# Optimization experiments

Hardware: AMD Instinct MI355X
Metric: run time of the kernel (lower is better)

The kernel has to match this reference:

```python
import jax, jax.numpy as jnp
import numpy as np

D_MODEL = 1024
HEADS = 16
D_HEAD = D_MODEL // HEADS


def setup_inputs() -> dict:
    key = jax.random.key(0)
    ks = jax.random.split(key, 7)
    s = 1.0 / np.sqrt(D_MODEL)
    x = jax.random.normal(ks[0], (4, 2048, D_MODEL), dtype=jnp.float32)
    Wq = jax.random.uniform(ks[1], (D_MODEL, D_MODEL), jnp.float32, -s, s)
    bq = jax.random.uniform(ks[2], (D_MODEL,), jnp.float32, -s, s)
    Wk = jax.random.uniform(ks[3], (D_MODEL, D_MODEL), jnp.float32, -s, s)
    bk = jax.random.uniform(ks[4], (D_MODEL,), jnp.float32, -s, s)
    Wv = jax.random.uniform(ks[5], (D_MODEL, D_MODEL), jnp.float32, -s, s)
    bv = jax.random.uniform(ks[6], (D_MODEL,), jnp.float32, -s, s)
    return {"x": x, "Wq": Wq, "bq": bq, "Wk": Wk, "bk": bk, "Wv": Wv, "bv": bv}


def reference(x, Wq, bq, Wk, bk, Wv, bv):
    B, S, D = x.shape
    # QKV projections, split heads: [B, H, S, Dh]
    def split(t):
        return t.reshape(B, S, HEADS, D_HEAD).transpose(0, 2, 1, 3)
    q = split(x @ Wq + bq)
    k = split(x @ Wk + bk)
    v = split(x @ Wv + bv)
    scores = jnp.einsum('bhqd,bhkd->bhqk', q, k) / np.sqrt(D_HEAD).astype(jnp.float32)
    attn = jax.nn.softmax(scores, axis=-1)
    out = jnp.einsum('bhqk,bhkd->bhqd', attn, v)
    return out.transpose(0, 2, 1, 3).reshape(B, S, D)
```

## Files before the change

kernel.cpp:

```cpp
#include <hip/hip_runtime.h>

typedef _Float16 f16;
typedef __attribute__((ext_vector_type(2))) _Float16 f16x2;
typedef __attribute__((ext_vector_type(2))) __fp16   hf16x2;
typedef __attribute__((ext_vector_type(4))) _Float16 f16x4;
typedef __attribute__((ext_vector_type(8))) _Float16 f16x8;
typedef __attribute__((ext_vector_type(4))) float    f32x4;

#define D_MODEL 1024
#define HEADS   16
#define DH      64
#define SEQ     2048
#define BATCH   4
#define SSCALE  0.1803368801111204f

__device__ __forceinline__ void gload_lds16(const void* g, void* lds) {
  __builtin_amdgcn_global_load_lds(
      (const __attribute__((address_space(1))) unsigned int*)g,
      (__attribute__((address_space(3))) unsigned int*)lds, 16, 0, 0);
}

__global__ __launch_bounds__(256) void prep_kernel(const float* __restrict__ x,
                                                   const float* __restrict__ Wq,
                                                   const float* __restrict__ Wk,
                                                   const float* __restrict__ Wv,
                                                   f16* __restrict__ xb,
                                                   f16* __restrict__ wt) {
  if (blockIdx.x < 8192) {
    int i = blockIdx.x * 256 + threadIdx.x;
    float4 v = ((const float4*)x)[i];
    f16x4 h;
    h[0] = (f16)v.x; h[1] = (f16)v.y; h[2] = (f16)v.z; h[3] = (f16)v.w;
    ((f16x4*)xb)[i] = h;
    return;
  }
  int bid = blockIdx.x - 8192;
  int z = bid >> 8, rem = bid & 255;
  const float* W = z == 0 ? Wq : (z == 1 ? Wk : Wv);
  f16* out = wt + (size_t)z * D_MODEL * D_MODEL;
  __shared__ float tile[64][65];
  int n0 = (rem & 15) * 64, k0 = (rem >> 4) * 64;
  int tx = threadIdx.x & 63, ty = threadIdx.x >> 6;
#pragma unroll
  for (int r = 0; r < 16; ++r)
    tile[ty * 16 + r][tx] = W[(size_t)(k0 + ty * 16 + r) * D_MODEL + n0 + tx];
  __syncthreads();
#pragma unroll
  for (int r = 0; r < 16; ++r)
    out[(size_t)(n0 + ty * 16 + r) * D_MODEL + k0 + tx] = (f16)tile[tx][ty * 16 + r];
}

__global__ __launch_bounds__(256, 3) void qkv_gemm_kernel(
    const f16* __restrict__ xb, const f16* __restrict__ wt_all,
    const float* __restrict__ bq, const float* __restrict__ bk, const float* __restrict__ bv,
    f16* __restrict__ qout, f16* __restrict__ kout, f16* __restrict__ vtout) {
  const int z = blockIdx.z;
  const f16* wt = wt_all + (size_t)z * D_MODEL * D_MODEL;
  const float* bias = z == 0 ? bq : (z == 1 ? bk : bv);
  const int n0 = blockIdx.x * 128, m0 = blockIdx.y * 128;

  __shared__ f16 As[2][128 * 32];
  __shared__ f16 Bs[2][128 * 32];

  const int tid = threadIdx.x;
  const int lane = tid & 63, w = tid >> 6;
  const int quad = lane >> 4, l15 = lane & 15;
  const int wm = w & 1, wn = w >> 1;

  const int pce = (quad ^ ((l15 >> 1) & 3)) * 8;
  const int aoff = wm * 2048 + l15 * 32 + pce;
  const int boff = wn * 2048 + l15 * 32 + pce;

  int srow[2], scl[2];
#pragma unroll
  for (int c = 0; c < 2; ++c) {
    int slot = (w * 2 + c) * 64 + lane;
    srow[c] = slot >> 2;
    scl[c] = (slot & 3) ^ ((srow[c] >> 1) & 3);
  }

  f32x4 acc[4][4];
#pragma unroll
  for (int i = 0; i < 4; ++i)
#pragma unroll
    for (int j = 0; j < 4; ++j) acc[i][j] = (f32x4){0.f, 0.f, 0.f, 0.f};

#pragma unroll
  for (int c = 0; c < 2; ++c) {
    gload_lds16(xb + (size_t)(m0 + srow[c]) * D_MODEL + scl[c] * 8, &As[0][(w * 2 + c) * 512]);
    gload_lds16(wt + (size_t)(n0 + srow[c]) * D_MODEL + scl[c] * 8, &Bs[0][(w * 2 + c) * 512]);
  }

  f16x8 aP[4], bP[4];
  for (int it = 0; it < 32; ++it) {
    const int buf = it & 1;
    __syncthreads();
    if (it < 31) {
      const int kn = (it + 1) * 32;
#pragma unroll
      for (int c = 0; c < 2; ++c) {
        gload_lds16(xb + (size_t)(m0 + srow[c]) * D_MODEL + kn + scl[c] * 8, &As[buf ^ 1][(w * 2 + c) * 512]);
        gload_lds16(wt + (size_t)(n0 + srow[c]) * D_MODEL + kn + scl[c] * 8, &Bs[buf ^ 1][(w * 2 + c) * 512]);
      }
    }
    f16x8 aC[4], bC[4];
#pragma unroll
    for (int mt = 0; mt < 4; ++mt) aC[mt] = *(const f16x8*)(&As[buf][aoff + mt * 512]);
#pragma unroll
    for (int nt = 0; nt < 4; ++nt) bC[nt] = *(const f16x8*)(&Bs[buf][boff + nt * 512]);
    if (it) {
#pragma unroll
      for (int mt = 0; mt < 4; ++mt)
#pragma unroll
        for (int nt = 0; nt < 4; ++nt)
          acc[mt][nt] = __builtin_amdgcn_mfma_f32_16x16x32_f16(aP[mt], bP[nt], acc[mt][nt], 0, 0, 0);
    }
#pragma unroll
    for (int t = 0; t < 4; ++t) { aP[t] = aC[t]; bP[t] = bC[t]; }
  }
#pragma unroll
  for (int mt = 0; mt < 4; ++mt)
#pragma unroll
    for (int nt = 0; nt < 4; ++nt)
      acc[mt][nt] = __builtin_amdgcn_mfma_f32_16x16x32_f16(aP[mt], bP[nt], acc[mt][nt], 0, 0, 0);

  const float sc = (z == 0) ? SSCALE : 1.0f;
  float bcol[4];
#pragma unroll
  for (int nt = 0; nt < 4; ++nt) bcol[nt] = bias[n0 + wn * 64 + nt * 16 + l15];

  if (z < 2) {
    f16* out = (z == 0) ? qout : kout;
#pragma unroll
    for (int mt = 0; mt < 4; ++mt) {
      int mbase = m0 + wm * 64 + mt * 16 + quad * 4;
#pragma unroll
      for (int nt = 0; nt < 4; ++nt) {
        int n = n0 + wn * 64 + nt * 16 + l15;
        int h = n >> 6, dh = n & 63;
#pragma unroll
        for (int r = 0; r < 4; ++r) {
          int m = mbase + r;
          int b = m >> 11, s = m & 2047;
          out[((size_t)(b * HEADS + h) * SEQ + s) * DH + dh] = (f16)((acc[mt][nt][r] + bcol[nt]) * sc);
        }
      }
    }
  } else {
#pragma unroll
    for (int mt = 0; mt < 4; ++mt) {
      int mbase = m0 + wm * 64 + mt * 16 + quad * 4;
      int b = mbase >> 11, seq = mbase & 2047;
      int kt = seq >> 6;
#pragma unroll
      for (int nt = 0; nt < 4; ++nt) {
        int n = n0 + wn * 64 + nt * 16 + l15;
        int h = n >> 6, dh = n & 63;
        f16x4 v;
#pragma unroll
        for (int r = 0; r < 4; ++r) v[r] = (f16)(acc[mt][nt][r] + bcol[nt]);
        int phys = (quad * 2 + (mt >> 1)) ^ (dh & 7);
        size_t off = (((size_t)(b * HEADS + h) * 32 + kt) * 4096) + dh * 64 + phys * 8 + (mt & 1) * 4;
        *(f16x4*)(vtout + off) = v;
      }
    }
  }
}

__global__ __launch_bounds__(256, 2) void attn_kernel(
    const f16* __restrict__ q, const f16* __restrict__ k, const f16* __restrict__ vt,
    float* __restrict__ out) {
  const int bh = blockIdx.x;
  const int s0 = blockIdx.y * 256;
  const int b = bh >> 4, h = bh & 15;
  const int tid = threadIdx.x, lane = tid & 63, w = tid >> 6;
  const int quad = lane >> 4, l15 = lane & 15;

  __shared__ f16 Ks[2][64 * 64];
  __shared__ f16 Vs[2][64 * 64];

  const f16* qbase = q + ((size_t)bh * SEQ + s0 + w * 64) * DH;
  const f16* kbase = k + (size_t)bh * SEQ * DH;
  const f16* vbase = vt + (size_t)bh * DH * SEQ;

  f16x8 qf[4][2];
#pragma unroll
  for (int qt = 0; qt < 4; ++qt)
#pragma unroll
    for (int ks = 0; ks < 2; ++ks)
      qf[qt][ks] = *(const f16x8*)(qbase + (qt * 16 + l15) * DH + ks * 32 + quad * 8);

  int koff[2];
  koff[0] = l15 * 64 + ((quad ^ (l15 & 7)) * 8);
  koff[1] = l15 * 64 + (((4 + quad) ^ (l15 & 7)) * 8);
  int voff2[2];
  voff2[0] = l15 * 64 + (((quad * 2) ^ (l15 & 7)) * 8);
  voff2[1] = l15 * 64 + (((quad * 2 + 1) ^ (l15 & 7)) * 8);

  int srow[2], scl[2];
#pragma unroll
  for (int c = 0; c < 2; ++c) {
    int slot = (w * 2 + c) * 64 + lane;
    srow[c] = slot >> 3;
    scl[c] = (slot & 7) ^ (srow[c] & 7);
  }
  const int vslot = ((w * 2) * 64 + lane) * 8;
  const int vslot2 = ((w * 2 + 1) * 64 + lane) * 8;

  f32x4 lsum4[4];
#pragma unroll
  for (int qt = 0; qt < 4; ++qt) lsum4[qt] = (f32x4){0.f, 0.f, 0.f, 0.f};
  f32x4 o[4][4];
#pragma unroll
  for (int i = 0; i < 4; ++i)
#pragma unroll
    for (int j = 0; j < 4; ++j) o[i][j] = (f32x4){0.f, 0.f, 0.f, 0.f};
  const f32x4 Zero = (f32x4){0.f, 0.f, 0.f, 0.f};

#pragma unroll
  for (int c = 0; c < 2; ++c)
    gload_lds16(kbase + (size_t)srow[c] * DH + scl[c] * 8, &Ks[0][(w * 2 + c) * 512]);
  gload_lds16(vbase + vslot,  &Vs[0][(w * 2) * 512]);
  gload_lds16(vbase + vslot2, &Vs[0][(w * 2 + 1) * 512]);

  for (int kt = 0; kt < SEQ / 64; ++kt) {
    const int buf = kt & 1;
    __syncthreads();
    if (kt < SEQ / 64 - 1) {
      const int kn = (kt + 1) * 64;
#pragma unroll
      for (int c = 0; c < 2; ++c)
        gload_lds16(kbase + (size_t)(kn + srow[c]) * DH + scl[c] * 8, &Ks[buf ^ 1][(w * 2 + c) * 512]);
      gload_lds16(vbase + (kt + 1) * 4096 + vslot,  &Vs[buf ^ 1][(w * 2) * 512]);
      gload_lds16(vbase + (kt + 1) * 4096 + vslot2, &Vs[buf ^ 1][(w * 2 + 1) * 512]);
    }

    f32x4 st[4][4];
#pragma unroll
    for (int mt = 0; mt < 4; ++mt) {
      f16x8 af0 = *(const f16x8*)(&Ks[buf][koff[0] + mt * 1024]);
      f16x8 af1 = *(const f16x8*)(&Ks[buf][koff[1] + mt * 1024]);
#pragma unroll
      for (int qt = 0; qt < 4; ++qt) {
        st[mt][qt] = __builtin_amdgcn_mfma_f32_16x16x32_f16(af0, qf[qt][0], Zero, 0, 0, 0);
        st[mt][qt] = __builtin_amdgcn_mfma_f32_16x16x32_f16(af1, qf[qt][1], st[mt][qt], 0, 0, 0);
      }
    }

    f16x4 pb[4][4];
#pragma unroll
    for (int ks = 0; ks < 4; ++ks)
#pragma unroll
      for (int qt = 0; qt < 4; ++qt) {
        float e0 = __builtin_amdgcn_exp2f(st[ks][qt][0]);
        float e1 = __builtin_amdgcn_exp2f(st[ks][qt][1]);
        float e2 = __builtin_amdgcn_exp2f(st[ks][qt][2]);
        float e3 = __builtin_amdgcn_exp2f(st[ks][qt][3]);
        f32x4 ev = (f32x4){e0, e1, e2, e3};
        lsum4[qt] += ev;
        f16x2 p01 = __builtin_bit_cast(f16x2, __builtin_amdgcn_cvt_pkrtz(e0, e1));
        f16x2 p23 = __builtin_bit_cast(f16x2, __builtin_amdgcn_cvt_pkrtz(e2, e3));
        pb[ks][qt] = __builtin_shufflevector(p01, p23, 0, 1, 2, 3);
      }

#pragma unroll
    for (int half = 0; half < 2; ++half)
#pragma unroll
      for (int mt = 0; mt < 4; ++mt) {
        f16x8 v8 = *(const f16x8*)(&Vs[buf][voff2[half] + mt * 1024]);
        f16x4 vaA = __builtin_shufflevector(v8, v8, 0, 1, 2, 3);
        f16x4 vaB = __builtin_shufflevector(v8, v8, 4, 5, 6, 7);
#pragma unroll
        for (int qt = 0; qt < 4; ++qt) {
          o[mt][qt] = __builtin_amdgcn_mfma_f32_16x16x16f16(vaA, pb[half * 2][qt], o[mt][qt], 0, 0, 0);
          o[mt][qt] = __builtin_amdgcn_mfma_f32_16x16x16f16(vaB, pb[half * 2 + 1][qt], o[mt][qt], 0, 0, 0);
        }
      }
  }

#pragma unroll
  for (int qt = 0; qt < 4; ++qt) {
    float l = (lsum4[qt][0] + lsum4[qt][1]) + (lsum4[qt][2] + lsum4[qt][3]);
    l += __shfl_xor(l, 16, 64);
    l += __shfl_xor(l, 32, 64);
    float inv = 1.f / l;
    int sq = s0 + w * 64 + qt * 16 + l15;
    float* obase = out + ((size_t)b * SEQ + sq) * D_MODEL + h * DH;
#pragma unroll
    for (int mt = 0; mt < 4; ++mt) {
      f32x4 vv;
#pragma unroll
      for (int r = 0; r < 4; ++r) vv[r] = o[mt][qt][r] * inv;
      *(f32x4*)(obase + mt * 16 + quad * 4) = vv;
    }
  }
}

extern "C" void kernel_launch(void* const* d_in, const int* in_sizes, int n_in,
                              void* d_out, int out_size, void* d_ws, size_t ws_size,
                              hipStream_t stream) {
  const float* x  = (const float*)d_in[0];
  const float* Wq = (const float*)d_in[1];
  const float* bq = (const float*)d_in[2];
  const float* Wk = (const float*)d_in[3];
  const float* bk = (const float*)d_in[4];
  const float* Wv = (const float*)d_in[5];
  const float* bv = (const float*)d_in[6];
  float* out = (float*)d_out;

  char* ws = (char*)d_ws;
  f16* xb = (f16*)ws;
  f16* wt = (f16*)(ws + (size_t)16 * 1024 * 1024);
  f16* q  = (f16*)(ws + (size_t)22 * 1024 * 1024);
  f16* kk = q + (size_t)BATCH * SEQ * D_MODEL;
  f16* vt = kk + (size_t)BATCH * SEQ * D_MODEL;

  prep_kernel<<<8192 + 768, 256, 0, stream>>>(x, Wq, Wk, Wv, xb, wt);
  qkv_gemm_kernel<<<dim3(8, 64, 3), 256, 0, stream>>>(xb, wt, bq, bk, bv, q, kk, vt);
  attn_kernel<<<dim3(64, 8), 256, 0, stream>>>(q, kk, vt, out);
}
```

Measured before the change: 246.7 us.

## Triple-buffer QKV GEMM loads and shrink attention query tile per wave

```diff
diff --git a/kernel.cpp b/kernel.cpp
--- a/kernel.cpp
+++ b/kernel.cpp
@@ -59,8 +59,8 @@
   const float* bias = z == 0 ? bq : (z == 1 ? bk : bv);
   const int n0 = blockIdx.x * 128, m0 = blockIdx.y * 128;
 
-  __shared__ f16 As[2][128 * 32];
-  __shared__ f16 Bs[2][128 * 32];
+  __shared__ f16 As[3][128 * 32];
+  __shared__ f16 Bs[3][128 * 32];
 
   const int tid = threadIdx.x;
   const int lane = tid & 63, w = tid >> 6;
@@ -86,21 +86,27 @@
     for (int j = 0; j < 4; ++j) acc[i][j] = (f32x4){0.f, 0.f, 0.f, 0.f};
 
 #pragma unroll
-  for (int c = 0; c < 2; ++c) {
-    gload_lds16(xb + (size_t)(m0 + srow[c]) * D_MODEL + scl[c] * 8, &As[0][(w * 2 + c) * 512]);
-    gload_lds16(wt + (size_t)(n0 + srow[c]) * D_MODEL + scl[c] * 8, &Bs[0][(w * 2 + c) * 512]);
-  }
+  for (int t = 0; t < 2; ++t)
+#pragma unroll
+    for (int c = 0; c < 2; ++c) {
+      gload_lds16(xb + (size_t)(m0 + srow[c]) * D_MODEL + t * 32 + scl[c] * 8, &As[t][(w * 2 + c) * 512]);
+      gload_lds16(wt + (size_t)(n0 + srow[c]) * D_MODEL + t * 32 + scl[c] * 8, &Bs[t][(w * 2 + c) * 512]);
+    }
 
   f16x8 aP[4], bP[4];
+  int buf = 0;
   for (int it = 0; it < 32; ++it) {
-    const int buf = it & 1;
-    __syncthreads();
-    if (it < 31) {
-      const int kn = (it + 1) * 32;
+    if (it == 31) { asm volatile("s_waitcnt vmcnt(0)" ::: "memory"); }
+    else          { asm volatile("s_waitcnt vmcnt(4)" ::: "memory"); }
+    __builtin_amdgcn_s_barrier();
+    __builtin_amdgcn_sched_barrier(0);
+    if (it < 30) {
+      const int sb = buf ? buf - 1 : 2;
+      const int kn = (it + 2) * 32;
 #pragma unroll
       for (int c = 0; c < 2; ++c) {
-        gload_lds16(xb + (size_t)(m0 + srow[c]) * D_MODEL + kn + scl[c] * 8, &As[buf ^ 1][(w * 2 + c) * 512]);
-        gload_lds16(wt + (size_t)(n0 + srow[c]) * D_MODEL + kn + scl[c] * 8, &Bs[buf ^ 1][(w * 2 + c) * 512]);
+        gload_lds16(xb + (size_t)(m0 + srow[c]) * D_MODEL + kn + scl[c] * 8, &As[sb][(w * 2 + c) * 512]);
+        gload_lds16(wt + (size_t)(n0 + srow[c]) * D_MODEL + kn + scl[c] * 8, &Bs[sb][(w * 2 + c) * 512]);
       }
     }
     f16x8 aC[4], bC[4];
@@ -117,6 +123,7 @@
     }
 #pragma unroll
     for (int t = 0; t < 4; ++t) { aP[t] = aC[t]; bP[t] = bC[t]; }
+    buf = (buf == 2) ? 0 : buf + 1;
   }
 #pragma unroll
   for (int mt = 0; mt < 4; ++mt)
@@ -167,11 +174,11 @@
   }
 }
 
-__global__ __launch_bounds__(256, 2) void attn_kernel(
+__global__ __launch_bounds__(256, 4) void attn_kernel(
     const f16* __restrict__ q, const f16* __restrict__ k, const f16* __restrict__ vt,
     float* __restrict__ out) {
   const int bh = blockIdx.x;
-  const int s0 = blockIdx.y * 256;
+  const int s0 = blockIdx.y * 128;
   const int b = bh >> 4, h = bh & 15;
   const int tid = threadIdx.x, lane = tid & 63, w = tid >> 6;
   const int quad = lane >> 4, l15 = lane & 15;
@@ -179,13 +186,13 @@
   __shared__ f16 Ks[2][64 * 64];
   __shared__ f16 Vs[2][64 * 64];
 
-  const f16* qbase = q + ((size_t)bh * SEQ + s0 + w * 64) * DH;
+  const f16* qbase = q + ((size_t)bh * SEQ + s0 + w * 32) * DH;
   const f16* kbase = k + (size_t)bh * SEQ * DH;
   const f16* vbase = vt + (size_t)bh * DH * SEQ;
 
-  f16x8 qf[4][2];
-#pragma unroll
-  for (int qt = 0; qt < 4; ++qt)
+  f16x8 qf[2][2];
+#pragma unroll
+  for (int qt = 0; qt < 2; ++qt)
 #pragma unroll
     for (int ks = 0; ks < 2; ++ks)
       qf[qt][ks] = *(const f16x8*)(qbase + (qt * 16 + l15) * DH + ks * 32 + quad * 8);
@@ -207,14 +214,14 @@
   const int vslot = ((w * 2) * 64 + lane) * 8;
   const int vslot2 = ((w * 2 + 1) * 64 + lane) * 8;
 
-  f32x4 lsum4[4];
-#pragma unroll
-  for (int qt = 0; qt < 4; ++qt) lsum4[qt] = (f32x4){0.f, 0.f, 0.f, 0.f};
-  f32x4 o[4][4];
+  f32x4 lsum4[2];
+#pragma unroll
+  for (int qt = 0; qt < 2; ++qt) lsum4[qt] = (f32x4){0.f, 0.f, 0.f, 0.f};
+  f32x4 o[4][2];
 #pragma unroll
   for (int i = 0; i < 4; ++i)
 #pragma unroll
-    for (int j = 0; j < 4; ++j) o[i][j] = (f32x4){0.f, 0.f, 0.f, 0.f};
+    for (int j = 0; j < 2; ++j) o[i][j] = (f32x4){0.f, 0.f, 0.f, 0.f};
   const f32x4 Zero = (f32x4){0.f, 0.f, 0.f, 0.f};
 
 #pragma unroll
@@ -235,33 +242,31 @@
       gload_lds16(vbase + (kt + 1) * 4096 + vslot2, &Vs[buf ^ 1][(w * 2 + 1) * 512]);
     }
 
-    f32x4 st[4][4];
+    f16x4 pb[4][2];
 #pragma unroll
     for (int mt = 0; mt < 4; ++mt) {
       f16x8 af0 = *(const f16x8*)(&Ks[buf][koff[0] + mt * 1024]);
       f16x8 af1 = *(const f16x8*)(&Ks[buf][koff[1] + mt * 1024]);
-#pragma unroll
-      for (int qt = 0; qt < 4; ++qt) {
-        st[mt][qt] = __builtin_amdgcn_mfma_f32_16x16x32_f16(af0, qf[qt][0], Zero, 0, 0, 0);
-        st[mt][qt] = __builtin_amdgcn_mfma_f32_16x16x32_f16(af1, qf[qt][1], st[mt][qt], 0, 0, 0);
-      }
-    }
-
-    f16x4 pb[4][4];
-#pragma unroll
-    for (int ks = 0; ks < 4; ++ks)
-#pragma unroll
-      for (int qt = 0; qt < 4; ++qt) {
-        float e0 = __builtin_amdgcn_exp2f(st[ks][qt][0]);
-        float e1 = __builtin_amdgcn_exp2f(st[ks][qt][1]);
-        float e2 = __builtin_amdgcn_exp2f(st[ks][qt][2]);
-        float e3 = __builtin_amdgcn_exp2f(st[ks][qt][3]);
+      __builtin_amdgcn_s_setprio(1);
+      f32x4 st0 = __builtin_amdgcn_mfma_f32_16x16x32_f16(af0, qf[0][0], Zero, 0, 0, 0);
+      st0 = __builtin_amdgcn_mfma_f32_16x16x32_f16(af1, qf[0][1], st0, 0, 0, 0);
+      f32x4 st1 = __builtin_amdgcn_mfma_f32_16x16x32_f16(af0, qf[1][0], Zero, 0, 0, 0);
+      st1 = __builtin_amdgcn_mfma_f32_16x16x32_f16(af1, qf[1][1], st1, 0, 0, 0);
+      __builtin_amdgcn_s_setprio(0);
+      f32x4 stv[2] = {st0, st1};
+#pragma unroll
+      for (int qt = 0; qt < 2; ++qt) {
+        float e0 = __builtin_amdgcn_exp2f(stv[qt][0]);
+        float e1 = __builtin_amdgcn_exp2f(stv[qt][1]);
+        float e2 = __builtin_amdgcn_exp2f(stv[qt][2]);
+        float e3 = __builtin_amdgcn_exp2f(stv[qt][3]);
         f32x4 ev = (f32x4){e0, e1, e2, e3};
         lsum4[qt] += ev;
         f16x2 p01 = __builtin_bit_cast(f16x2, __builtin_amdgcn_cvt_pkrtz(e0, e1));
         f16x2 p23 = __builtin_bit_cast(f16x2, __builtin_amdgcn_cvt_pkrtz(e2, e3));
-        pb[ks][qt] = __builtin_shufflevector(p01, p23, 0, 1, 2, 3);
-      }
+        pb[mt][qt] = __builtin_shufflevector(p01, p23, 0, 1, 2, 3);
+      }
+    }
 
 #pragma unroll
     for (int half = 0; half < 2; ++half)
@@ -270,21 +275,23 @@
         f16x8 v8 = *(const f16x8*)(&Vs[buf][voff2[half] + mt * 1024]);
         f16x4 vaA = __builtin_shufflevector(v8, v8, 0, 1, 2, 3);
         f16x4 vaB = __builtin_shufflevector(v8, v8, 4, 5, 6, 7);
-#pragma unroll
-        for (int qt = 0; qt < 4; ++qt) {
+        __builtin_amdgcn_s_setprio(1);
+#pragma unroll
+        for (int qt = 0; qt < 2; ++qt) {
           o[mt][qt] = __builtin_amdgcn_mfma_f32_16x16x16f16(vaA, pb[half * 2][qt], o[mt][qt], 0, 0, 0);
           o[mt][qt] = __builtin_amdgcn_mfma_f32_16x16x16f16(vaB, pb[half * 2 + 1][qt], o[mt][qt], 0, 0, 0);
         }
-      }
-  }
-
-#pragma unroll
-  for (int qt = 0; qt < 4; ++qt) {
+        __builtin_amdgcn_s_setprio(0);
+      }
+  }
+
+#pragma unroll
+  for (int qt = 0; qt < 2; ++qt) {
     float l = (lsum4[qt][0] + lsum4[qt][1]) + (lsum4[qt][2] + lsum4[qt][3]);
     l += __shfl_xor(l, 16, 64);
     l += __shfl_xor(l, 32, 64);
     float inv = 1.f / l;
-    int sq = s0 + w * 64 + qt * 16 + l15;
+    int sq = s0 + w * 32 + qt * 16 + l15;
     float* obase = out + ((size_t)b * SEQ + sq) * D_MODEL + h * DH;
 #pragma unroll
     for (int mt = 0; mt < 4; ++mt) {
@@ -317,5 +324,5 @@
 
   prep_kernel<<<8192 + 768, 256, 0, stream>>>(x, Wq, Wk, Wv, xb, wt);
   qkv_gemm_kernel<<<dim3(8, 64, 3), 256, 0, stream>>>(xb, wt, bq, bk, bv, q, kk, vt);
-  attn_kernel<<<dim3(64, 8), 256, 0, stream>>>(q, kk, vt, out);
-}
+  attn_kernel<<<dim3(64, 16), 256, 0, stream>>>(q, kk, vt, out);
+}
```

After: 248.1 us. Within noise of the previous version (+0.6%).
